# Kernel optimization log

Measured on AMD Instinct MI355X. Metric: run time of the kernel, lower is better.

## Reference

```python
import jax, jax.numpy as jnp
import numpy as np

VOCAB, EMBED, HIDDEN = 256, 512, 1024
B, T = 64, 512


def setup_inputs() -> dict:
    key = jax.random.key(0)
    ks = jax.random.split(key, 12)
    s = 0.02
    return {
        "x": jax.random.randint(ks[0], (B, T), 0, VOCAB),
        "embed": jax.random.normal(ks[1], (VOCAB, EMBED), jnp.float32) * s,
        "Wih0": jax.random.normal(ks[2], (3 * HIDDEN, EMBED), jnp.float32) * s,
        "Whh0": jax.random.normal(ks[3], (3 * HIDDEN, HIDDEN), jnp.float32) * s,
        "bih0": jax.random.normal(ks[4], (3 * HIDDEN,), jnp.float32) * s,
        "bhh0": jax.random.normal(ks[5], (3 * HIDDEN,), jnp.float32) * s,
        "Wih1": jax.random.normal(ks[6], (3 * HIDDEN, HIDDEN), jnp.float32) * s,
        "Whh1": jax.random.normal(ks[7], (3 * HIDDEN, HIDDEN), jnp.float32) * s,
        "bih1": jax.random.normal(ks[8], (3 * HIDDEN,), jnp.float32) * s,
        "bhh1": jax.random.normal(ks[9], (3 * HIDDEN,), jnp.float32) * s,
        "W_out": jax.random.normal(ks[10], (VOCAB, HIDDEN), jnp.float32) * s,
        "b_out": jax.random.normal(ks[11], (VOCAB,), jnp.float32) * s,
    }


def gru_cell(inp, h, Wih, Whh, bih, bhh):
    # PyTorch GRUCell math.
    gi = inp @ Wih.T + bih  # (B, 3H)
    gh = h @ Whh.T + bhh    # (B, 3H)
    i_r, i_z, i_n = jnp.split(gi, 3, axis=-1)
    h_r, h_z, h_n = jnp.split(gh, 3, axis=-1)
    r = jax.nn.sigmoid(i_r + h_r)
    z = jax.nn.sigmoid(i_z + h_z)
    n = jnp.tanh(i_n + r * h_n)
    return (1.0 - z) * n + z * h


def reference(x, embed, Wih0, Whh0, bih0, bhh0, Wih1, Whh1, bih1, bhh1, W_out, b_out):
    emb = embed[x]                       # (B, T, E)
    xs = jnp.swapaxes(emb, 0, 1)         # (T, B, E)
    h0 = jnp.zeros((x.shape[0], HIDDEN), emb.dtype)

    def step(carry, inp_t):
        h_0, h_1 = carry
        h_0 = gru_cell(inp_t, h_0, Wih0, Whh0, bih0, bhh0)
        h_1 = gru_cell(h_0, h_1, Wih1, Whh1, bih1, bhh1)
        return (h_0, h_1), h_1

    _, outs = jax.lax.scan(step, (h0, h0), xs)   # outs: (T, B, H)
    outs = jnp.swapaxes(outs, 0, 1)              # (B, T, H)
    logits = outs @ W_out.T + b_out              # (B, T, V)
    return logits
```

## Files before the change

### kernel.cpp

```cpp
#include <hip/hip_runtime.h>
#include <stdint.h>

typedef short short8 __attribute__((ext_vector_type(8)));
typedef float f32x4 __attribute__((ext_vector_type(4)));
typedef unsigned short u16;

#define MFMA16(a, b, c) __builtin_amdgcn_mfma_f32_16x16x32_bf16((a), (b), (c), 0, 0, 0)

#define T_LEN 512
#define BATCH 64
#define EMB_D 512
#define HID 1024
#define VOC 256
#define NWG 128
#define RNN_THREADS 512
#define RING 128
#define SLOT (BATCH * HID)

#define OFF_XT    0u
#define OFF_EMBT  131072u
#define OFF_WIH0  524288u
#define OFF_WHH0  3670016u
#define OFF_WIH1  9961472u
#define OFF_WHH1  16252928u
#define OFF_WOUT  22544384u
#define OFF_H0R   23068672u
#define OFF_H1R   39845888u
#define OFF_H1ALL 56623104u
#define OFF_SYNC  123731968u
#define SYNC_BYTES 16640u
#define WS_TOTAL  (OFF_SYNC + SYNC_BYTES)

static __device__ __forceinline__ u16 f2b(float f) {
  uint32_t u = __float_as_uint(f);
  u += 0x7FFFu + ((u >> 16) & 1u);
  return (u16)(u >> 16);
}
static __device__ __forceinline__ float sigm(float x) { return 1.0f / (1.0f + __expf(-x)); }

__global__ void cvt_kernel(const float* __restrict__ src, u16* __restrict__ dst, int n) {
  int i = ((int)blockIdx.x * 256 + (int)threadIdx.x) * 4;
  if (i + 4 <= n) {
    const float4 v = *(const float4*)(src + i);
    ushort4 o;
    o.x = f2b(v.x); o.y = f2b(v.y); o.z = f2b(v.z); o.w = f2b(v.w);
    *(ushort4*)(dst + i) = o;
  }
}

__global__ void xt_kernel(const int* __restrict__ x, int* __restrict__ xT) {
  const int t = (int)blockIdx.x, b = (int)threadIdx.x;
  xT[t * BATCH + b] = x[b * T_LEN + t];
}

__global__ __launch_bounds__(RNN_THREADS, 1) void rnn_persist_kernel(
    const int* __restrict__ xT, const u16* __restrict__ embtab,
    const u16* __restrict__ A0i_r, const u16* __restrict__ A0i_z, const u16* __restrict__ A0i_n,
    const u16* __restrict__ A0h_r, const u16* __restrict__ A0h_z, const u16* __restrict__ A0h_n,
    const u16* __restrict__ A1i_r, const u16* __restrict__ A1i_z, const u16* __restrict__ A1i_n,
    const u16* __restrict__ A1h_r, const u16* __restrict__ A1h_z, const u16* __restrict__ A1h_n,
    const float* __restrict__ bih0, const float* __restrict__ bhh0,
    const float* __restrict__ bih1, const float* __restrict__ bhh1,
    u16* __restrict__ h0r, u16* __restrict__ h1r,
    u16* __restrict__ h1all, unsigned* __restrict__ flags)
{
  __shared__ __align__(16) float lds[16384];
  const int tid = (int)threadIdx.x;
  const int wv = tid >> 6;
  const int lane = tid & 63;
  const int lrow = lane & 15;
  const int lk8 = (lane >> 4) << 3;
  const int wgid = (int)blockIdx.x;
  const int layer = wgid >> 6;
  const int ubase = (wgid & 63) << 4;
  const bool iwave = (wv < 4);
  const bool l0i = (layer == 0) && iwave;

  const u16 *Ar, *Az, *An;
  int ldb, k0;
  if (layer == 0) {
    if (iwave) { Ar = A0i_r; Az = A0i_z; An = A0i_n; ldb = EMB_D; k0 = wv * 128; }
    else       { Ar = A0h_r; Az = A0h_z; An = A0h_n; ldb = HID;   k0 = (wv - 4) * 256; }
  } else {
    if (iwave) { Ar = A1i_r; Az = A1i_z; An = A1i_n; ldb = HID;   k0 = wv * 256; }
    else       { Ar = A1h_r; Az = A1h_z; An = A1h_n; ldb = HID;   k0 = (wv - 4) * 256; }
  }
  const size_t arow = (size_t)(ubase + lrow) * ldb;

  const float* bi = layer ? bih1 : bih0;
  const float* bh = layer ? bhh1 : bhh0;
  const int u0 = (tid & 7) * 2;
  const int eb = tid >> 3;
  const int eug0 = ubase + u0, eug1 = eug0 + 1;
  const float bR0 = bi[eug0] + bh[eug0];
  const float bZ0 = bi[HID + eug0] + bh[HID + eug0];
  const float bNi0 = bi[2 * HID + eug0];
  const float bNh0 = bh[2 * HID + eug0];
  const float bR1 = bi[eug1] + bh[eug1];
  const float bZ1 = bi[HID + eug1] + bh[HID + eug1];
  const float bNi1 = bi[2 * HID + eug1];
  const float bNh1 = bh[2 * HID + eug1];
  const int l_e = ((u0 >> 2) << 4) | (eb & 15);
  const int r0 = u0 & 3, r1 = r0 + 1;
  const int ebt = eb >> 4;
  const int ix0 = l_e ^ (r0 << 3), ix1 = l_e ^ (r1 << 3);
  float hp0 = 0.f, hp1 = 0.f;

  for (int s = 0; s <= T_LEN; ++s) {
    const bool active = (layer == 0) ? (s < T_LEN) : (s >= 1);
    if (active) {
      const u16* h0prev = h0r + (size_t)((s - 1) & (RING - 1)) * SLOT;
      const u16* h1prev = h1r + (size_t)((s - 2) & (RING - 1)) * SLOT;

      f32x4 acc0[4], acc1[4], accn[4];
#pragma unroll
      for (int bt = 0; bt < 4; ++bt) {
        acc0[bt] = (f32x4){0.f, 0.f, 0.f, 0.f};
        acc1[bt] = (f32x4){0.f, 0.f, 0.f, 0.f};
        accn[bt] = (f32x4){0.f, 0.f, 0.f, 0.f};
      }
      if (l0i) {
        const u16* brow[4];
#pragma unroll
        for (int bt = 0; bt < 4; ++bt) {
          const int tok = xT[s * BATCH + bt * 16 + lrow];
          brow[bt] = embtab + (size_t)tok * EMB_D;
        }
#pragma unroll
        for (int ks = 0; ks < 4; ++ks) {
          const int kk = k0 + ks * 32 + lk8;
          const short8 ar = *(const short8*)(Ar + arow + kk);
          const short8 az = *(const short8*)(Az + arow + kk);
          const short8 an = *(const short8*)(An + arow + kk);
          const short8 b0 = *(const short8*)(brow[0] + kk);
          const short8 b1 = *(const short8*)(brow[1] + kk);
          const short8 b2 = *(const short8*)(brow[2] + kk);
          const short8 b3 = *(const short8*)(brow[3] + kk);
          acc0[0] = MFMA16(ar, b0, acc0[0]); acc1[0] = MFMA16(az, b0, acc1[0]); accn[0] = MFMA16(an, b0, accn[0]);
          acc0[1] = MFMA16(ar, b1, acc0[1]); acc1[1] = MFMA16(az, b1, acc1[1]); accn[1] = MFMA16(an, b1, accn[1]);
          acc0[2] = MFMA16(ar, b2, acc0[2]); acc1[2] = MFMA16(az, b2, acc1[2]); accn[2] = MFMA16(an, b2, accn[2]);
          acc0[3] = MFMA16(ar, b3, acc0[3]); acc1[3] = MFMA16(az, b3, acc1[3]); accn[3] = MFMA16(an, b3, accn[3]);
        }
      } else {
        const u16* Bp;
        if (layer == 0) Bp = h0prev;
        else            Bp = iwave ? h0prev : h1prev;
#pragma unroll
        for (int ks = 0; ks < 8; ++ks) {
          const int kk = k0 + ks * 32 + lk8;
          const short8 ar = *(const short8*)(Ar + arow + kk);
          const short8 az = *(const short8*)(Az + arow + kk);
          const short8 an = *(const short8*)(An + arow + kk);
#pragma unroll
          for (int bt = 0; bt < 4; ++bt) {
            const short8 bf = *(const short8*)(Bp + (size_t)(bt * 16 + lrow) * HID + kk);
            acc0[bt] = MFMA16(ar, bf, acc0[bt]);
            acc1[bt] = MFMA16(az, bf, acc1[bt]);
            accn[bt] = MFMA16(an, bf, accn[bt]);
          }
        }
      }
      if (iwave) {
#pragma unroll
        for (int bt = 0; bt < 4; ++bt)
#pragma unroll
          for (int r = 0; r < 4; ++r) {
            const int ix = lane ^ (r << 3);
            lds[(((wv * 4 + 0) * 4 + bt) * 256) + r * 64 + ix] = acc0[bt][r];
            lds[(((wv * 4 + 1) * 4 + bt) * 256) + r * 64 + ix] = acc1[bt][r];
            lds[(((wv * 4 + 2) * 4 + bt) * 256) + r * 64 + ix] = accn[bt][r];
          }
      }
      __syncthreads();
      if (!iwave) {
        const int z = wv - 4;
#pragma unroll
        for (int bt = 0; bt < 4; ++bt)
#pragma unroll
          for (int r = 0; r < 4; ++r) {
            const int ix = lane ^ (r << 3);
            float* p0 = &lds[(((z * 4 + 0) * 4 + bt) * 256) + r * 64 + ix];
            float* p1 = &lds[(((z * 4 + 1) * 4 + bt) * 256) + r * 64 + ix];
            *p0 = *p0 + acc0[bt][r];
            *p1 = *p1 + acc1[bt][r];
            lds[(((z * 4 + 3) * 4 + bt) * 256) + r * 64 + ix] = accn[bt][r];
          }
      }
      __syncthreads();
      {
        float sr0 = 0.f, sz0 = 0.f, sni0 = 0.f, snh0 = 0.f;
        float sr1 = 0.f, sz1 = 0.f, sni1 = 0.f, snh1 = 0.f;
#pragma unroll
        for (int z = 0; z < 4; ++z) {
          sr0  += lds[(((z * 4 + 0) * 4 + ebt) * 256) + r0 * 64 + ix0];
          sz0  += lds[(((z * 4 + 1) * 4 + ebt) * 256) + r0 * 64 + ix0];
          sni0 += lds[(((z * 4 + 2) * 4 + ebt) * 256) + r0 * 64 + ix0];
          snh0 += lds[(((z * 4 + 3) * 4 + ebt) * 256) + r0 * 64 + ix0];
          sr1  += lds[(((z * 4 + 0) * 4 + ebt) * 256) + r1 * 64 + ix1];
          sz1  += lds[(((z * 4 + 1) * 4 + ebt) * 256) + r1 * 64 + ix1];
          sni1 += lds[(((z * 4 + 2) * 4 + ebt) * 256) + r1 * 64 + ix1];
          snh1 += lds[(((z * 4 + 3) * 4 + ebt) * 256) + r1 * 64 + ix1];
        }
        const float rg0 = sigm(sr0 + bR0);
        const float zg0 = sigm(sz0 + bZ0);
        const float ng0 = tanhf(sni0 + bNi0 + rg0 * (snh0 + bNh0));
        const float hn0 = (1.0f - zg0) * ng0 + zg0 * hp0;
        const float rg1 = sigm(sr1 + bR1);
        const float zg1 = sigm(sz1 + bZ1);
        const float ng1 = tanhf(sni1 + bNi1 + rg1 * (snh1 + bNh1));
        const float hn1 = (1.0f - zg1) * ng1 + zg1 * hp1;
        hp0 = hn0; hp1 = hn1;
        const unsigned packed = (unsigned)f2b(hn0) | ((unsigned)f2b(hn1) << 16);
        u16* wslot = layer ? (h1r + (size_t)((s - 1) & (RING - 1)) * SLOT)
                           : (h0r + (size_t)(s & (RING - 1)) * SLOT);
        __hip_atomic_store((unsigned*)&wslot[eb * HID + eug0], packed,
                           __ATOMIC_RELAXED, __HIP_MEMORY_SCOPE_AGENT);
        if (layer)
          *(unsigned*)&h1all[((size_t)(s - 1) * BATCH + eb) * HID + eug0] = packed;
      }
    }
    if (s < T_LEN) {
      __syncthreads();
      const unsigned ep = (unsigned)(s + 1);
      if (tid == 0)
        __hip_atomic_store(&flags[wgid * 32], ep, __ATOMIC_RELAXED, __HIP_MEMORY_SCOPE_AGENT);
      if (tid < NWG) {
        while (__hip_atomic_load(&flags[tid * 32], __ATOMIC_RELAXED,
                                 __HIP_MEMORY_SCOPE_AGENT) < ep)
          __builtin_amdgcn_s_sleep(1);
      }
      __syncthreads();
    }
  }
}

__global__ __launch_bounds__(256, 2) void logits_kernel(
    const u16* __restrict__ h1all, const u16* __restrict__ Woutb,
    const float* __restrict__ bout, float* __restrict__ out)
{
  __shared__ __align__(16) short lds[16 * 4 * 64 * 8];
  const int tid = (int)threadIdx.x;
  const int wv = tid >> 6, lane = tid & 63;
  const int lrow = lane & 15, lk8 = (lane >> 4) << 3;
  const int row0 = (int)blockIdx.x * 64 + wv * 16;
  f32x4 acc[16];
#pragma unroll
  for (int i = 0; i < 16; ++i) acc[i] = (f32x4){0.f, 0.f, 0.f, 0.f};

  for (int kc = 0; kc < HID; kc += 128) {
    __syncthreads();
#pragma unroll
    for (int j = 0; j < 16; ++j) {
      const int slot = tid + j * 256;
      const int ct = slot >> 8, kt = (slot >> 6) & 3, l = slot & 63;
      *(short8*)&lds[slot * 8] =
          *(const short8*)(Woutb + (size_t)(ct * 16 + (l & 15)) * HID + kc + kt * 32 + ((l >> 4) << 3));
    }
    __syncthreads();
#pragma unroll
    for (int kt = 0; kt < 4; ++kt) {
      const short8 af = *(const short8*)(h1all + (size_t)(row0 + lrow) * HID + kc + kt * 32 + lk8);
#pragma unroll
      for (int ct = 0; ct < 16; ++ct) {
        const short8 bf = *(const short8*)&lds[((ct * 4 + kt) * 64 + lane) * 8];
        acc[ct] = MFMA16(af, bf, acc[ct]);
      }
    }
  }
#pragma unroll
  for (int ct = 0; ct < 16; ++ct) {
    const int v = ct * 16 + lrow;
    const float bo = bout[v];
#pragma unroll
    for (int r = 0; r < 4; ++r) {
      const int row = row0 + (lane >> 4) * 4 + r;
      const int t = row >> 6, b = row & 63;
      out[((size_t)(b * T_LEN + t)) * VOC + v] = acc[ct][r] + bo;
    }
  }
}

extern "C" void kernel_launch(void* const* d_in, const int* in_sizes, int n_in,
                              void* d_out, int out_size, void* d_ws, size_t ws_size,
                              hipStream_t stream) {
  const int*   x     = (const int*)d_in[0];
  const float* embed = (const float*)d_in[1];
  const float* Wih0  = (const float*)d_in[2];
  const float* Whh0  = (const float*)d_in[3];
  const float* bih0  = (const float*)d_in[4];
  const float* bhh0  = (const float*)d_in[5];
  const float* Wih1  = (const float*)d_in[6];
  const float* Whh1  = (const float*)d_in[7];
  const float* bih1  = (const float*)d_in[8];
  const float* bhh1  = (const float*)d_in[9];
  const float* Wout  = (const float*)d_in[10];
  const float* bout  = (const float*)d_in[11];
  float* out = (float*)d_out;
  char* ws = (char*)d_ws;
  if (ws_size < (size_t)WS_TOTAL) return;

  hipMemsetAsync(ws + OFF_H0R + (size_t)(RING - 1) * SLOT * 2, 0, SLOT * 2, stream);
  hipMemsetAsync(ws + OFF_H1R + (size_t)(RING - 1) * SLOT * 2, 0, SLOT * 2, stream);
  hipMemsetAsync(ws + OFF_SYNC, 0, SYNC_BYTES, stream);
  xt_kernel<<<512, 64, 0, stream>>>(x, (int*)(ws + OFF_XT));
  cvt_kernel<<<128, 256, 0, stream>>>(embed, (u16*)(ws + OFF_EMBT), 256 * 512);
  cvt_kernel<<<1536, 256, 0, stream>>>(Wih0, (u16*)(ws + OFF_WIH0), 3072 * 512);
  cvt_kernel<<<3072, 256, 0, stream>>>(Whh0, (u16*)(ws + OFF_WHH0), 3072 * 1024);
  cvt_kernel<<<3072, 256, 0, stream>>>(Wih1, (u16*)(ws + OFF_WIH1), 3072 * 1024);
  cvt_kernel<<<3072, 256, 0, stream>>>(Whh1, (u16*)(ws + OFF_WHH1), 3072 * 1024);
  cvt_kernel<<<256, 256, 0, stream>>>(Wout, (u16*)(ws + OFF_WOUT), 256 * 1024);

  const u16* wih0b = (const u16*)(ws + OFF_WIH0);
  const u16* whh0b = (const u16*)(ws + OFF_WHH0);
  const u16* wih1b = (const u16*)(ws + OFF_WIH1);
  const u16* whh1b = (const u16*)(ws + OFF_WHH1);

  rnn_persist_kernel<<<NWG, RNN_THREADS, 0, stream>>>(
      (const int*)(ws + OFF_XT), (const u16*)(ws + OFF_EMBT),
      wih0b, wih0b + 524288, wih0b + 1048576,
      whh0b, whh0b + 1048576, whh0b + 2097152,
      wih1b, wih1b + 1048576, wih1b + 2097152,
      whh1b, whh1b + 1048576, whh1b + 2097152,
      bih0, bhh0, bih1, bhh1,
      (u16*)(ws + OFF_H0R), (u16*)(ws + OFF_H1R),
      (u16*)(ws + OFF_H1ALL), (unsigned*)(ws + OFF_SYNC));

  logits_kernel<<<512, 256, 0, stream>>>((const u16*)(ws + OFF_H1ALL),
                                         (const u16*)(ws + OFF_WOUT), bout, out);
}
```

Measured before the change: 7.838 ms.

## Replace global all-WG barrier with per-layer producer-consumer flags and deeper h0 ring

Swaps the per-step grid-wide barrier across all 128 workgroups for split flag arrays per layer. Layer-0 groups now wait only on their own layer's previous step, plus a loose backpressure check on layer 1 so the ring is not overwritten. Layer-1 groups wait on layer 0 at step s and layer 1 at step s-1. The h0 ring grows to 256 slots and the h1 ring shrinks to 8, which lets layer 0 run ahead of layer 1 and keeps one layer's stalls from blocking the other. The risk is correctness of the ring-distance and backpressure logic, and layer 0 running far ahead may add memory traffic.

Result: no change. 7.787 ms (-0.6%).

```diff
diff --git a/kernel.cpp b/kernel.cpp
--- a/kernel.cpp
+++ b/kernel.cpp
@@ -14,7 +14,8 @@
 #define VOC 256
 #define NWG 128
 #define RNN_THREADS 512
-#define RING 128
+#define R0 256
+#define R1 8
 #define SLOT (BATCH * HID)
 
 #define OFF_XT    0u
@@ -25,9 +26,9 @@
 #define OFF_WHH1  16252928u
 #define OFF_WOUT  22544384u
 #define OFF_H0R   23068672u
-#define OFF_H1R   39845888u
-#define OFF_H1ALL 56623104u
-#define OFF_SYNC  123731968u
+#define OFF_H1R   56623104u
+#define OFF_H1ALL 57671680u
+#define OFF_SYNC  124780544u
 #define SYNC_BYTES 16640u
 #define WS_TOTAL  (OFF_SYNC + SYNC_BYTES)
 
@@ -51,6 +52,17 @@
 __global__ void xt_kernel(const int* __restrict__ x, int* __restrict__ xT) {
   const int t = (int)blockIdx.x, b = (int)threadIdx.x;
   xT[t * BATCH + b] = x[b * T_LEN + t];
+}
+
+static __device__ __forceinline__ void poll_flags(unsigned* p0, unsigned* p1,
+                                                  unsigned t0, unsigned t1, int tid) {
+  if (tid < 128) {
+    unsigned* f = (tid < 64) ? (p0 + (size_t)tid * 32) : (p1 + (size_t)(tid - 64) * 32);
+    const unsigned tgt = (tid < 64) ? t0 : t1;
+    while (__hip_atomic_load(f, __ATOMIC_RELAXED, __HIP_MEMORY_SCOPE_AGENT) < tgt)
+      __builtin_amdgcn_s_sleep(1);
+  }
+  __syncthreads();
 }
 
 __global__ __launch_bounds__(RNN_THREADS, 1) void rnn_persist_kernel(
@@ -62,7 +74,7 @@
     const float* __restrict__ bih0, const float* __restrict__ bhh0,
     const float* __restrict__ bih1, const float* __restrict__ bhh1,
     u16* __restrict__ h0r, u16* __restrict__ h1r,
-    u16* __restrict__ h1all, unsigned* __restrict__ flags)
+    u16* __restrict__ h1all, unsigned* __restrict__ sync)
 {
   __shared__ __align__(16) float lds[16384];
   const int tid = (int)threadIdx.x;
@@ -75,6 +87,8 @@
   const int ubase = (wgid & 63) << 4;
   const bool iwave = (wv < 4);
   const bool l0i = (layer == 0) && iwave;
+  unsigned* p0 = sync;
+  unsigned* p1 = sync + 64 * 32;
 
   const u16 *Ar, *Az, *An;
   int ldb, k0;
@@ -106,11 +120,20 @@
   const int ix0 = l_e ^ (r0 << 3), ix1 = l_e ^ (r1 << 3);
   float hp0 = 0.f, hp1 = 0.f;
 
-  for (int s = 0; s <= T_LEN; ++s) {
-    const bool active = (layer == 0) ? (s < T_LEN) : (s >= 1);
-    if (active) {
-      const u16* h0prev = h0r + (size_t)((s - 1) & (RING - 1)) * SLOT;
-      const u16* h1prev = h1r + (size_t)((s - 2) & (RING - 1)) * SLOT;
+  const int sBeg = (layer == 0) ? 0 : 1;
+  const int sEnd = (layer == 0) ? (T_LEN - 1) : T_LEN;
+
+  for (int s = sBeg; s <= sEnd; ++s) {
+    if (layer == 0) {
+      const unsigned bp = (s >= 252) ? (unsigned)(s - 250) : 0u;
+      poll_flags(p0, p1, (unsigned)s, bp, tid);
+    } else {
+      poll_flags(p0, p1, (unsigned)s, (unsigned)(s - 1), tid);
+    }
+
+    {
+      const u16* h0prev = h0r + (size_t)((s - 1) & (R0 - 1)) * SLOT;
+      const u16* h1prev = h1r + (size_t)((s - 2) & (R1 - 1)) * SLOT;
 
       f32x4 acc0[4], acc1[4], accn[4];
 #pragma unroll
@@ -179,10 +202,10 @@
 #pragma unroll
           for (int r = 0; r < 4; ++r) {
             const int ix = lane ^ (r << 3);
-            float* p0 = &lds[(((z * 4 + 0) * 4 + bt) * 256) + r * 64 + ix];
-            float* p1 = &lds[(((z * 4 + 1) * 4 + bt) * 256) + r * 64 + ix];
-            *p0 = *p0 + acc0[bt][r];
-            *p1 = *p1 + acc1[bt][r];
+            float* q0 = &lds[(((z * 4 + 0) * 4 + bt) * 256) + r * 64 + ix];
+            float* q1 = &lds[(((z * 4 + 1) * 4 + bt) * 256) + r * 64 + ix];
+            *q0 = *q0 + acc0[bt][r];
+            *q1 = *q1 + acc1[bt][r];
             lds[(((z * 4 + 3) * 4 + bt) * 256) + r * 64 + ix] = accn[bt][r];
           }
       }
@@ -211,25 +234,19 @@
         const float hn1 = (1.0f - zg1) * ng1 + zg1 * hp1;
         hp0 = hn0; hp1 = hn1;
         const unsigned packed = (unsigned)f2b(hn0) | ((unsigned)f2b(hn1) << 16);
-        u16* wslot = layer ? (h1r + (size_t)((s - 1) & (RING - 1)) * SLOT)
-                           : (h0r + (size_t)(s & (RING - 1)) * SLOT);
+        u16* wslot = layer ? (h1r + (size_t)((s - 1) & (R1 - 1)) * SLOT)
+                           : (h0r + (size_t)(s & (R0 - 1)) * SLOT);
         __hip_atomic_store((unsigned*)&wslot[eb * HID + eug0], packed,
                            __ATOMIC_RELAXED, __HIP_MEMORY_SCOPE_AGENT);
         if (layer)
           *(unsigned*)&h1all[((size_t)(s - 1) * BATCH + eb) * HID + eug0] = packed;
       }
     }
-    if (s < T_LEN) {
-      __syncthreads();
-      const unsigned ep = (unsigned)(s + 1);
-      if (tid == 0)
-        __hip_atomic_store(&flags[wgid * 32], ep, __ATOMIC_RELAXED, __HIP_MEMORY_SCOPE_AGENT);
-      if (tid < NWG) {
-        while (__hip_atomic_load(&flags[tid * 32], __ATOMIC_RELAXED,
-                                 __HIP_MEMORY_SCOPE_AGENT) < ep)
-          __builtin_amdgcn_s_sleep(1);
-      }
-      __syncthreads();
+    __syncthreads();
+    if (tid == 0) {
+      unsigned* f = layer ? (p1 + (size_t)(wgid - 64) * 32) : (p0 + (size_t)wgid * 32);
+      __hip_atomic_store(f, (unsigned)(s + (layer ? 0 : 1)), __ATOMIC_RELAXED,
+                         __HIP_MEMORY_SCOPE_AGENT);
     }
   }
 }
@@ -299,8 +316,8 @@
   char* ws = (char*)d_ws;
   if (ws_size < (size_t)WS_TOTAL) return;
 
-  hipMemsetAsync(ws + OFF_H0R + (size_t)(RING - 1) * SLOT * 2, 0, SLOT * 2, stream);
-  hipMemsetAsync(ws + OFF_H1R + (size_t)(RING - 1) * SLOT * 2, 0, SLOT * 2, stream);
+  hipMemsetAsync(ws + OFF_H0R + (size_t)(R0 - 1) * SLOT * 2, 0, SLOT * 2, stream);
+  hipMemsetAsync(ws + OFF_H1R + (size_t)(R1 - 1) * SLOT * 2, 0, SLOT * 2, stream);
   hipMemsetAsync(ws + OFF_SYNC, 0, SYNC_BYTES, stream);
   xt_kernel<<<512, 64, 0, stream>>>(x, (int*)(ws + OFF_XT));
   cvt_kernel<<<128, 256, 0, stream>>>(embed, (u16*)(ws + OFF_EMBT), 256 * 512);
```
